# Kernel tuning notes

Measured on AMD Instinct MI355X. Metric: run time of the kernel, lower is better.

Reference implementation:

```python
import jax, jax.numpy as jnp
import numpy as np

B, C, D, H, W = 2, 64, 20, 20, 20
RATIO = 8
CQ = C // RATIO  # Q/K channels = 8


def setup_inputs() -> dict:
    key = jax.random.key(0)
    ks = jax.random.split(key, 8)
    s = 0.05
    return {
        "x": jax.random.normal(ks[0], (B, C, D, H, W), dtype=jnp.float32),
        "Wq": jax.random.normal(ks[1], (CQ, C), dtype=jnp.float32) * s,
        "bq": jax.random.normal(ks[2], (CQ,), dtype=jnp.float32) * s,
        "Wk": jax.random.normal(ks[3], (CQ, C), dtype=jnp.float32) * s,
        "bk": jax.random.normal(ks[4], (CQ,), dtype=jnp.float32) * s,
        "Wv": jax.random.normal(ks[5], (C, C), dtype=jnp.float32) * s,
        "bv": jax.random.normal(ks[6], (C,), dtype=jnp.float32) * s,
        "gamma": jax.random.normal(ks[7], (1,), dtype=jnp.float32) * s,
    }


def reference(x, Wq, bq, Wk, bk, Wv, bv, gamma):
    b, c, *spatial = x.shape
    n = int(np.prod(spatial))
    xf = x.reshape(b, c, n)  # [B, C, N]
    # 1x1 convs == per-position channel matmuls
    Q = jnp.einsum('oc,bcn->bon', Wq, xf) + bq[None, :, None]  # [B, Cq, N]
    K = jnp.einsum('oc,bcn->bon', Wk, xf) + bk[None, :, None]  # [B, Cq, N]
    V = jnp.einsum('oc,bcn->bon', Wv, xf) + bv[None, :, None]  # [B, C, N]
    # energy[b, n, m] = sum_q Q[b, q, n] * K[b, q, m]  (no scaling, as in source)
    energy = jnp.einsum('bqn,bqm->bnm', Q, K)  # [B, N, N]
    attention = jax.nn.softmax(energy, axis=-1)
    # out[b, c, n] = sum_m V[b, c, m] * attention[b, n, m]
    out = jnp.einsum('bcm,bnm->bcn', V, attention)
    out = out.reshape(b, c, *spatial)
    return gamma * out + x
```

## Files before the change

kernel.cpp:

```cpp
#include <hip/hip_runtime.h>
#include <hip/hip_bf16.h>

#define BB 2
#define CC 64
#define CQk 8
#define NN 8000
#define TB 256
#define QT 4
#define NWAVE 8
#define NBLK32 250

using f32x4  = __attribute__((ext_vector_type(4))) float;
using bf16x8 = __attribute__((ext_vector_type(8))) short;
typedef unsigned short ushort_t;

__device__ __forceinline__ ushort_t f2bf(float f) {
    __hip_bfloat16 h = __float2bfloat16(f);
    return *reinterpret_cast<ushort_t*>(&h);
}

__global__ void detect_dtype(const void* __restrict__ x, int* __restrict__ flag)
{
    const float* xf = (const float*)x;
    const int t = threadIdx.x;
    const float a = fabsf(xf[t * 8]);
    const int ok = (a > 9.765625e-4f && a < 16.0f) ? 1 : 0;
    const unsigned long long m = __ballot(ok);
    if (t == 0) flag[0] = (__popcll(m) >= 48) ? 1 : 0;
}

__device__ __forceinline__ float loadF(const void* p, size_t i, int isf) {
    return isf ? ((const float*)p)[i]
               : __bfloat162float(((const __hip_bfloat16*)p)[i]);
}

__device__ __forceinline__ int vidx(int n) {
    const int h = (n & 15) >> 2;
    const int i = (n & 3) + (((n >> 4) & 1) << 2);
    return (n & ~31) + h * 8 + i;
}

__global__ __launch_bounds__(TB) void qkv_kernel(
    const void* __restrict__ x,
    const void* __restrict__ Wq, const void* __restrict__ bq,
    const void* __restrict__ Wk, const void* __restrict__ bk,
    const void* __restrict__ Wv, const void* __restrict__ bv,
    ushort_t* __restrict__ Qbf, ushort_t* __restrict__ Kbf,
    ushort_t* __restrict__ Vtp, const int* __restrict__ flag)
{
    __shared__ float sW[16][CC];
    __shared__ float sB[16];
    const int isf = flag[0];
    const int t = threadIdx.x;
    const int chunk = blockIdx.y;

    for (int i = t; i < 16 * CC; i += TB) {
        const int rr = i >> 6, c = i & 63;
        const int r = chunk * 16 + rr;
        float w;
        if (r < CQk)          w = loadF(Wq, (size_t)r * CC + c, isf);
        else if (r < 2 * CQk) w = loadF(Wk, (size_t)(r - CQk) * CC + c, isf);
        else                  w = loadF(Wv, (size_t)(r - 2 * CQk) * CC + c, isf);
        sW[rr][c] = w;
    }
    if (t < 16) {
        const int r = chunk * 16 + t;
        float bias;
        if (r < CQk)          bias = loadF(bq, r, isf);
        else if (r < 2 * CQk) bias = loadF(bk, r - CQk, isf);
        else                  bias = loadF(bv, r - 2 * CQk, isf);
        sB[t] = bias;
    }
    __syncthreads();

    const int pos = blockIdx.x * TB + t;
    if (pos >= BB * NN) return;
    const int b = pos / NN, n = pos % NN;

    float xv[CC];
    const size_t xbase = (size_t)b * CC * NN + n;
#pragma unroll
    for (int c = 0; c < CC; ++c) xv[c] = loadF(x, xbase + (size_t)c * NN, isf);

    float acc[16];
#pragma unroll
    for (int rr = 0; rr < 16; ++rr) {
        float a = sB[rr];
#pragma unroll
        for (int c = 0; c < CC; ++c) a += sW[rr][c] * xv[c];
        acc[rr] = a;
    }

    const size_t pn = (size_t)b * NN + n;
    if (chunk == 0) {
        bf16x8 pq, pk;
#pragma unroll
        for (int j = 0; j < 8; ++j) {
            pq[j] = (short)f2bf(acc[j] * 1.44269504089f);
            pk[j] = (short)f2bf(acc[8 + j]);
        }
        *(bf16x8*)&Qbf[pn * 8] = pq;
        *(bf16x8*)&Kbf[pn * 8] = pk;
    } else {
        const int c0 = (chunk - 1) * 16;
        const int vn = vidx(n);
#pragma unroll
        for (int rr = 0; rr < 16; ++rr)
            Vtp[((size_t)b * CC + c0 + rr) * NN + vn] = f2bf(acc[rr]);
    }
}

__global__ __launch_bounds__(512) void attn_fused(
    const ushort_t* __restrict__ Qbf, const ushort_t* __restrict__ Kbf,
    const ushort_t* __restrict__ Vtp,
    const void* __restrict__ x, const void* __restrict__ gamma,
    void* __restrict__ out, const int* __restrict__ flag)
{
    __shared__ float sO[64][65];
    __shared__ float sL[64];
    const int isf = flag[0];
    const int tid = threadIdx.x;
    const int lane = tid & 63;
    const int w = tid >> 6;
    const int cl = lane & 15, h = lane >> 4;
    const int q0 = blockIdx.x * 64;
    const int b = blockIdx.y;
    const size_t bN = (size_t)b * NN;

    for (int i = tid; i < 64 * 65; i += 512) (&sO[0][0])[i] = 0.f;
    if (tid < 64) sL[tid] = 0.f;
    __syncthreads();

    bf16x8 qb[QT];
#pragma unroll
    for (int t = 0; t < QT; ++t) {
        bf16x8 z;
#pragma unroll
        for (int j = 0; j < 8; ++j) z[j] = 0;
        if (h == 0) z = *(const bf16x8*)&Qbf[(bN + q0 + t * 16 + cl) * 8];
        qb[t] = z;
    }

    bf16x8 ones;
#pragma unroll
    for (int j = 0; j < 8; ++j) ones[j] = (short)0x3F80;

    const f32x4 zf = {0.f, 0.f, 0.f, 0.f};
    f32x4 acc[QT][4];
    f32x4 lac[QT];
#pragma unroll
    for (int t = 0; t < QT; ++t) {
        lac[t] = zf;
#pragma unroll
        for (int ct = 0; ct < 4; ++ct) acc[t][ct] = zf;
    }

    for (int bi = w; bi < NBLK32; bi += NWAVE) {
        const int m0 = bi * 32;

        bf16x8 ka0, ka1;
#pragma unroll
        for (int j = 0; j < 8; ++j) { ka0[j] = 0; ka1[j] = 0; }
        if (h == 0) {
            ka0 = *(const bf16x8*)&Kbf[(bN + m0 + cl) * 8];
            ka1 = *(const bf16x8*)&Kbf[(bN + m0 + 16 + cl) * 8];
        }

        bf16x8 vb[4];
#pragma unroll
        for (int ct = 0; ct < 4; ++ct)
            vb[ct] = *(const bf16x8*)&Vtp[((size_t)b * CC + ct * 16 + cl) * NN + m0 + h * 8];

#pragma unroll
        for (int t = 0; t < QT; ++t) {
            f32x4 e0 = __builtin_amdgcn_mfma_f32_16x16x32_bf16(ka0, qb[t], zf, 0, 0, 0);
            f32x4 e1 = __builtin_amdgcn_mfma_f32_16x16x32_bf16(ka1, qb[t], zf, 0, 0, 0);
            bf16x8 af;
#pragma unroll
            for (int r = 0; r < 4; ++r) {
                af[r]     = (short)f2bf(exp2f(e0[r]));
                af[4 + r] = (short)f2bf(exp2f(e1[r]));
            }
#pragma unroll
            for (int ct = 0; ct < 4; ++ct)
                acc[t][ct] = __builtin_amdgcn_mfma_f32_16x16x32_bf16(af, vb[ct], acc[t][ct], 0, 0, 0);
            lac[t] = __builtin_amdgcn_mfma_f32_16x16x32_bf16(af, ones, lac[t], 0, 0, 0);
        }
    }

#pragma unroll
    for (int t = 0; t < QT; ++t) {
#pragma unroll
        for (int ct = 0; ct < 4; ++ct)
#pragma unroll
            for (int r = 0; r < 4; ++r)
                atomicAdd(&sO[t * 16 + 4 * h + r][ct * 16 + cl], acc[t][ct][r]);
        if (cl == 0) {
#pragma unroll
            for (int r = 0; r < 4; ++r)
                atomicAdd(&sL[t * 16 + 4 * h + r], lac[t][r]);
        }
    }
    __syncthreads();

    const float g = loadF(gamma, 0, isf);
    const int qq = tid & 63;
    const int crow = tid >> 6;
    const float rL = 1.0f / sL[qq];
#pragma unroll
    for (int p = 0; p < 8; ++p) {
        const int c = p * 8 + crow;
        const size_t idx = ((size_t)b * CC + c) * NN + q0 + qq;
        const float val = g * sO[qq][c] * rL + loadF(x, idx, isf);
        if (isf) ((float*)out)[idx] = val;
        else     ((__hip_bfloat16*)out)[idx] = __float2bfloat16(val);
    }
}

extern "C" void kernel_launch(void* const* d_in, const int* in_sizes, int n_in,
                              void* d_out, int out_size, void* d_ws, size_t ws_size,
                              hipStream_t stream)
{
    const void* x     = d_in[0];
    const void* Wq    = d_in[1];
    const void* bq    = d_in[2];
    const void* Wk    = d_in[3];
    const void* bk    = d_in[4];
    const void* Wv    = d_in[5];
    const void* bv    = d_in[6];
    const void* gamma = d_in[7];

    char* base = (char*)d_ws;
    int* flag = (int*)base;
    size_t off = 256;
    ushort_t* Qbf = (ushort_t*)(base + off); off += (size_t)BB * NN * CQk * 2;
    ushort_t* Kbf = (ushort_t*)(base + off); off += (size_t)BB * NN * CQk * 2;
    ushort_t* Vtp = (ushort_t*)(base + off); off += ((size_t)BB * CC * NN + 64) * 2;

    detect_dtype<<<1, 64, 0, stream>>>(x, flag);

    dim3 g1((BB * NN + TB - 1) / TB, 5);
    qkv_kernel<<<g1, TB, 0, stream>>>(x, Wq, bq, Wk, bk, Wv, bv, Qbf, Kbf, Vtp, flag);

    dim3 g2(NN / 64, BB);
    attn_fused<<<g2, 512, 0, stream>>>(Qbf, Kbf, Vtp, x, gamma, d_out, flag);
}
```

Before: 112.4 us.

## Merge QKV chunks into one pass, prefetch K/V tiles, and use fast exp2 with bf16 packing

The QKV kernel now computes all 80 output rows per thread in a single launch instead of five chunk launches. Each x column is therefore read once rather than five times, at the cost of more shared memory and registers per thread. The attention loop software-prefetches the next K/V tile into registers while computing the current one, which should hide global load latency. It also swaps exp2f for the hardware exp2 builtin and converts pairs of values to bf16 with a simple add-and-shift rounding pack. That pack is cheaper but does not handle NaN specially and is not exact round-to-nearest-even.

```diff
diff --git a/kernel.cpp b/kernel.cpp
--- a/kernel.cpp
+++ b/kernel.cpp
@@ -5,7 +5,7 @@
 #define CC 64
 #define CQk 8
 #define NN 8000
-#define TB 256
+#define QKV_TB 128
 #define QT 4
 #define NWAVE 8
 #define NBLK32 250
@@ -13,10 +13,25 @@
 using f32x4  = __attribute__((ext_vector_type(4))) float;
 using bf16x8 = __attribute__((ext_vector_type(8))) short;
 typedef unsigned short ushort_t;
+typedef unsigned int uint_t;
 
 __device__ __forceinline__ ushort_t f2bf(float f) {
     __hip_bfloat16 h = __float2bfloat16(f);
     return *reinterpret_cast<ushort_t*>(&h);
+}
+
+__device__ __forceinline__ float exp2_fast(float x) {
+#if __has_builtin(__builtin_amdgcn_exp2f)
+    return __builtin_amdgcn_exp2f(x);
+#else
+    return exp2f(x);
+#endif
+}
+
+__device__ __forceinline__ uint_t pack_bf16(float a, float b) {
+    const uint_t ua = __builtin_bit_cast(uint_t, a) + 0x8000u;
+    const uint_t ub = __builtin_bit_cast(uint_t, b) + 0x8000u;
+    return (ua >> 16) | (ub & 0xFFFF0000u);
 }
 
 __global__ void detect_dtype(const void* __restrict__ x, int* __restrict__ flag)
@@ -40,7 +55,7 @@
     return (n & ~31) + h * 8 + i;
 }
 
-__global__ __launch_bounds__(TB) void qkv_kernel(
+__global__ __launch_bounds__(QKV_TB) void qkv_kernel(
     const void* __restrict__ x,
     const void* __restrict__ Wq, const void* __restrict__ bq,
     const void* __restrict__ Wk, const void* __restrict__ bk,
@@ -48,32 +63,29 @@
     ushort_t* __restrict__ Qbf, ushort_t* __restrict__ Kbf,
     ushort_t* __restrict__ Vtp, const int* __restrict__ flag)
 {
-    __shared__ float sW[16][CC];
-    __shared__ float sB[16];
+    __shared__ float sW[80][CC];
+    __shared__ float sB[80];
     const int isf = flag[0];
     const int t = threadIdx.x;
-    const int chunk = blockIdx.y;
-
-    for (int i = t; i < 16 * CC; i += TB) {
-        const int rr = i >> 6, c = i & 63;
-        const int r = chunk * 16 + rr;
+
+    for (int i = t; i < 80 * CC; i += QKV_TB) {
+        const int r = i >> 6, c = i & 63;
         float w;
         if (r < CQk)          w = loadF(Wq, (size_t)r * CC + c, isf);
         else if (r < 2 * CQk) w = loadF(Wk, (size_t)(r - CQk) * CC + c, isf);
         else                  w = loadF(Wv, (size_t)(r - 2 * CQk) * CC + c, isf);
-        sW[rr][c] = w;
-    }
-    if (t < 16) {
-        const int r = chunk * 16 + t;
+        sW[r][c] = w;
+    }
+    if (t < 80) {
         float bias;
-        if (r < CQk)          bias = loadF(bq, r, isf);
-        else if (r < 2 * CQk) bias = loadF(bk, r - CQk, isf);
-        else                  bias = loadF(bv, r - 2 * CQk, isf);
+        if (t < CQk)          bias = loadF(bq, t, isf);
+        else if (t < 2 * CQk) bias = loadF(bk, t - CQk, isf);
+        else                  bias = loadF(bv, t - 2 * CQk, isf);
         sB[t] = bias;
     }
     __syncthreads();
 
-    const int pos = blockIdx.x * TB + t;
+    const int pos = blockIdx.x * QKV_TB + t;
     if (pos >= BB * NN) return;
     const int b = pos / NN, n = pos % NN;
 
@@ -82,17 +94,16 @@
 #pragma unroll
     for (int c = 0; c < CC; ++c) xv[c] = loadF(x, xbase + (size_t)c * NN, isf);
 
-    float acc[16];
-#pragma unroll
-    for (int rr = 0; rr < 16; ++rr) {
-        float a = sB[rr];
-#pragma unroll
-        for (int c = 0; c < CC; ++c) a += sW[rr][c] * xv[c];
-        acc[rr] = a;
-    }
-
     const size_t pn = (size_t)b * NN + n;
-    if (chunk == 0) {
+    {
+        float acc[16];
+#pragma unroll
+        for (int rr = 0; rr < 16; ++rr) {
+            float a = sB[rr];
+#pragma unroll
+            for (int c = 0; c < CC; ++c) a += sW[rr][c] * xv[c];
+            acc[rr] = a;
+        }
         bf16x8 pq, pk;
 #pragma unroll
         for (int j = 0; j < 8; ++j) {
@@ -101,12 +112,21 @@
         }
         *(bf16x8*)&Qbf[pn * 8] = pq;
         *(bf16x8*)&Kbf[pn * 8] = pk;
-    } else {
-        const int c0 = (chunk - 1) * 16;
-        const int vn = vidx(n);
+    }
+    const int vn = vidx(n);
+#pragma unroll
+    for (int g = 0; g < 4; ++g) {
+        float acc[16];
+#pragma unroll
+        for (int rr = 0; rr < 16; ++rr) {
+            float a = sB[16 + g * 16 + rr];
+#pragma unroll
+            for (int c = 0; c < CC; ++c) a += sW[16 + g * 16 + rr][c] * xv[c];
+            acc[rr] = a;
+        }
 #pragma unroll
         for (int rr = 0; rr < 16; ++rr)
-            Vtp[((size_t)b * CC + c0 + rr) * NN + vn] = f2bf(acc[rr]);
+            Vtp[((size_t)b * CC + g * 16 + rr) * NN + vn] = f2bf(acc[rr]);
     }
 }
 
@@ -131,12 +151,13 @@
     if (tid < 64) sL[tid] = 0.f;
     __syncthreads();
 
+    bf16x8 zero8;
+#pragma unroll
+    for (int j = 0; j < 8; ++j) zero8[j] = 0;
     bf16x8 qb[QT];
 #pragma unroll
     for (int t = 0; t < QT; ++t) {
-        bf16x8 z;
-#pragma unroll
-        for (int j = 0; j < 8; ++j) z[j] = 0;
+        bf16x8 z = zero8;
         if (h == 0) z = *(const bf16x8*)&Qbf[(bN + q0 + t * 16 + cl) * 8];
         qb[t] = z;
     }
@@ -155,37 +176,55 @@
         for (int ct = 0; ct < 4; ++ct) acc[t][ct] = zf;
     }
 
-    for (int bi = w; bi < NBLK32; bi += NWAVE) {
-        const int m0 = bi * 32;
-
-        bf16x8 ka0, ka1;
-#pragma unroll
-        for (int j = 0; j < 8; ++j) { ka0[j] = 0; ka1[j] = 0; }
+    const ushort_t* Vb = Vtp + (size_t)b * CC * NN;
+
+    bf16x8 ka0 = zero8, ka1 = zero8, vb0, vb1, vb2, vb3;
+    {
+        const int m0 = w * 32;
         if (h == 0) {
             ka0 = *(const bf16x8*)&Kbf[(bN + m0 + cl) * 8];
             ka1 = *(const bf16x8*)&Kbf[(bN + m0 + 16 + cl) * 8];
         }
-
-        bf16x8 vb[4];
-#pragma unroll
-        for (int ct = 0; ct < 4; ++ct)
-            vb[ct] = *(const bf16x8*)&Vtp[((size_t)b * CC + ct * 16 + cl) * NN + m0 + h * 8];
+        const size_t vo = (size_t)cl * NN + m0 + h * 8;
+        vb0 = *(const bf16x8*)&Vb[vo];
+        vb1 = *(const bf16x8*)&Vb[16 * NN + vo];
+        vb2 = *(const bf16x8*)&Vb[32 * NN + vo];
+        vb3 = *(const bf16x8*)&Vb[48 * NN + vo];
+    }
+
+    for (int bi = w; bi < NBLK32; bi += NWAVE) {
+        const int pb = (bi + NWAVE < NBLK32) ? (bi + NWAVE) : bi;
+        const int pm0 = pb * 32;
+        bf16x8 nka0 = zero8, nka1 = zero8, nvb0, nvb1, nvb2, nvb3;
+        if (h == 0) {
+            nka0 = *(const bf16x8*)&Kbf[(bN + pm0 + cl) * 8];
+            nka1 = *(const bf16x8*)&Kbf[(bN + pm0 + 16 + cl) * 8];
+        }
+        {
+            const size_t vo = (size_t)cl * NN + pm0 + h * 8;
+            nvb0 = *(const bf16x8*)&Vb[vo];
+            nvb1 = *(const bf16x8*)&Vb[16 * NN + vo];
+            nvb2 = *(const bf16x8*)&Vb[32 * NN + vo];
+            nvb3 = *(const bf16x8*)&Vb[48 * NN + vo];
+        }
 
 #pragma unroll
         for (int t = 0; t < QT; ++t) {
             f32x4 e0 = __builtin_amdgcn_mfma_f32_16x16x32_bf16(ka0, qb[t], zf, 0, 0, 0);
             f32x4 e1 = __builtin_amdgcn_mfma_f32_16x16x32_bf16(ka1, qb[t], zf, 0, 0, 0);
-            bf16x8 af;
-#pragma unroll
-            for (int r = 0; r < 4; ++r) {
-                af[r]     = (short)f2bf(exp2f(e0[r]));
-                af[4 + r] = (short)f2bf(exp2f(e1[r]));
-            }
-#pragma unroll
-            for (int ct = 0; ct < 4; ++ct)
-                acc[t][ct] = __builtin_amdgcn_mfma_f32_16x16x32_bf16(af, vb[ct], acc[t][ct], 0, 0, 0);
-            lac[t] = __builtin_amdgcn_mfma_f32_16x16x32_bf16(af, ones, lac[t], 0, 0, 0);
-        }
+            union { uint_t u[4]; bf16x8 v; } afu;
+            afu.u[0] = pack_bf16(exp2_fast(e0[0]), exp2_fast(e0[1]));
+            afu.u[1] = pack_bf16(exp2_fast(e0[2]), exp2_fast(e0[3]));
+            afu.u[2] = pack_bf16(exp2_fast(e1[0]), exp2_fast(e1[1]));
+            afu.u[3] = pack_bf16(exp2_fast(e1[2]), exp2_fast(e1[3]));
+            const bf16x8 af = afu.v;
+            acc[t][0] = __builtin_amdgcn_mfma_f32_16x16x32_bf16(af, vb0, acc[t][0], 0, 0, 0);
+            acc[t][1] = __builtin_amdgcn_mfma_f32_16x16x32_bf16(af, vb1, acc[t][1], 0, 0, 0);
+            acc[t][2] = __builtin_amdgcn_mfma_f32_16x16x32_bf16(af, vb2, acc[t][2], 0, 0, 0);
+            acc[t][3] = __builtin_amdgcn_mfma_f32_16x16x32_bf16(af, vb3, acc[t][3], 0, 0, 0);
+            lac[t]    = __builtin_amdgcn_mfma_f32_16x16x32_bf16(af, ones, lac[t], 0, 0, 0);
+        }
+        ka0 = nka0; ka1 = nka1; vb0 = nvb0; vb1 = nvb1; vb2 = nvb2; vb3 = nvb3;
     }
 
 #pragma unroll
@@ -239,8 +278,8 @@
 
     detect_dtype<<<1, 64, 0, stream>>>(x, flag);
 
-    dim3 g1((BB * NN + TB - 1) / TB, 5);
-    qkv_kernel<<<g1, TB, 0, stream>>>(x, Wq, bq, Wk, bk, Wv, bv, Qbf, Kbf, Vtp, flag);
+    dim3 g1((BB * NN + QKV_TB - 1) / QKV_TB);
+    qkv_kernel<<<g1, QKV_TB, 0, stream>>>(x, Wq, bq, Wk, bk, Wv, bv, Qbf, Kbf, Vtp, flag);
 
     dim3 g2(NN / 64, BB);
     attn_fused<<<g2, 512, 0, stream>>>(Qbf, Kbf, Vtp, x, gamma, d_out, flag);
```

Result: slower. 144.2 us (+28.3%).
